# Optimization experiments

Hardware: AMD Instinct MI355X
Metric: run time of the kernel (lower is better)

Reference implementation:

```python
import jax, jax.numpy as jnp
import numpy as np

B, S, H = 8, 1024, 768
NUM_HEADS, DH = 12, 64
A, T = 12, 64

def setup_inputs() -> dict:
    key = jax.random.key(0)
    ks = jax.random.split(key, 12)
    all_tokens = jax.random.normal(ks[0], (B, S, H), dtype=jnp.float32)
    aspect_tokens = jax.random.normal(ks[1], (B, A, H), dtype=jnp.float32)
    # ragged target slices: start in [0, S-17), length in [1, 16]
    starts = jax.random.randint(ks[2], (T,), 0, S - 17)
    lens = jax.random.randint(ks[3], (T,), 1, 17)
    target_pos_info = jnp.stack([starts, starts + lens], axis=-1).astype(jnp.int32)  # (T,2)
    target_batch_info = jnp.sort(jax.random.randint(ks[4], (T,), 0, B)).astype(jnp.int32)
    attention_mask = jnp.ones((B, S), dtype=jnp.int32)
    s = 0.02
    W1 = jax.random.normal(ks[5], (H, H), dtype=jnp.float32) * s
    b1 = jnp.zeros((H,), dtype=jnp.float32)
    Wq = jax.random.normal(ks[6], (H, NUM_HEADS, DH), dtype=jnp.float32) * s
    bq = jnp.zeros((NUM_HEADS, DH), dtype=jnp.float32)
    Wk = jax.random.normal(ks[7], (H, NUM_HEADS, DH), dtype=jnp.float32) * s
    bk = jnp.zeros((NUM_HEADS, DH), dtype=jnp.float32)
    Wc = jax.random.normal(ks[8], (2 * H, 1), dtype=jnp.float32) * s
    bc = jnp.zeros((1,), dtype=jnp.float32)
    return {"all_tokens": all_tokens, "aspect_tokens": aspect_tokens,
            "target_pos_info": target_pos_info, "target_batch_info": target_batch_info,
            "attention_mask": attention_mask,
            "W1": W1, "b1": b1, "Wq": Wq, "bq": bq, "Wk": Wk, "bk": bk,
            "Wc": Wc, "bc": bc}


def reference(all_tokens, aspect_tokens, target_pos_info, target_batch_info,
              attention_mask, W1, b1, Wq, bq, Wk, bk, Wc, bc):
    # linear_transform (shared for tokens and aspects), dropout = identity at eval
    h = jax.nn.relu(jnp.einsum('bsh,hg->bsg', all_tokens, W1) + b1)     # (B,S,H)
    # SelfAttention: q/k EinsumDense projections; value = raw key_states reshaped
    q = jnp.einsum('bsh,hkd->bskd', h, Wq) + bq                          # (B,S,K,D)
    k = jnp.einsum('bsh,hkd->bskd', h, Wk) + bk
    v = h.reshape(k.shape)                                               # faithful: reshape, no proj
    q = q * jax.lax.rsqrt(jnp.asarray(DH, q.dtype))
    scores = jnp.einsum('bskd,bqkd->bkqs', k, q)                         # (B,K,Q,S)
    mask_val = attention_mask[:, 0].astype(scores.dtype)                 # original uses mask[:, 0:1]
    scores = scores + ((1.0 - mask_val) * -10000.0)[:, None, None, None]
    probs = jax.nn.softmax(scores, axis=-1)
    out = jnp.einsum('bkqs,bskd->bqkd', probs, v).reshape(h.shape)       # (B,S,H)
    # ragged per-target slice mean: masked mean over positions [s0, s1)
    pos = jnp.arange(S)
    s0, s1 = target_pos_info[:, 0], target_pos_info[:, 1]
    span = ((pos[None, :] >= s0[:, None]) & (pos[None, :] < s1[:, None])).astype(out.dtype)  # (T,S)
    gathered = out[target_batch_info]                                    # (T,S,H)
    counts = jnp.maximum(span.sum(-1, keepdims=True), 1.0)
    rep = jnp.einsum('ts,tsh->th', span, gathered) / counts              # (T,H)
    # aspect hidden states and target-aspect pairing (batch-ordered concat)
    h_a = jax.nn.relu(jnp.einsum('bah,hg->bag', aspect_tokens, W1) + b1)  # (B,A,H)
    pair = jnp.concatenate([jnp.broadcast_to(rep[:, None, :], (rep.shape[0], A, H)),
                            h_a[target_batch_info]], axis=-1)             # (T,A,2H)
    t_a_logit = jnp.einsum('tac,co->tao', pair, Wc) + bc                  # (T,A,1)
    return t_a_logit
```

## Files before the change

### kernel.cpp

```cpp
#include <hip/hip_runtime.h>


typedef __attribute__((ext_vector_type(8))) short s8v;
typedef __attribute__((ext_vector_type(4))) short s4v;
typedef __attribute__((ext_vector_type(4))) float f4v;

#define AS1 __attribute__((address_space(1)))
#define AS3 __attribute__((address_space(3)))

__device__ __forceinline__ unsigned short f2bf(float f) {
  union { float f; unsigned u; } v; v.f = f;
  unsigned r = v.u + 0x7FFFu + ((v.u >> 16) & 1u);
  return (unsigned short)(r >> 16);
}

__device__ __forceinline__ float bf2f(unsigned short u) {
  union { unsigned u; float f; } v; v.u = ((unsigned)u) << 16;
  return v.f;
}

__device__ __forceinline__ void gl2lds16(const void* g, void* l) {
  __builtin_amdgcn_global_load_lds((const AS1 void*)g, (AS3 void*)l, 16, 0, 0);
}

__global__ __launch_bounds__(256) void k_prep(const float* __restrict__ asp,
                                              const float* __restrict__ W1,
                                              const float* __restrict__ Wq,
                                              const float* __restrict__ Wk,
                                              unsigned short* __restrict__ Abf,
                                              unsigned short* __restrict__ W1t,
                                              unsigned short* __restrict__ Wqt,
                                              unsigned short* __restrict__ Wkt,
                                              float* __restrict__ outz) {
  __shared__ float T[64][68];
  int bid = blockIdx.x;
  int tid = threadIdx.x;
  if (bid < 36) {
    int i = bid * 256 + tid;
    const float4* src = (const float4*)(asp + (size_t)i * 8);
    float4 a = src[0], b = src[1];
    s8v o;
    o[0] = (short)f2bf(a.x); o[1] = (short)f2bf(a.y);
    o[2] = (short)f2bf(a.z); o[3] = (short)f2bf(a.w);
    o[4] = (short)f2bf(b.x); o[5] = (short)f2bf(b.y);
    o[6] = (short)f2bf(b.z); o[7] = (short)f2bf(b.w);
    *(s8v*)(Abf + (size_t)i * 8) = o;
  } else if (bid < 468) {
    int wb = bid - 36;
    const float* W = (wb < 144) ? W1 : (wb < 288) ? Wq : Wk;
    unsigned short* Wt = (wb < 144) ? W1t : (wb < 288) ? Wqt : Wkt;
    int tile = wb % 144;
    int tr = (tile / 12) * 64;
    int tc = (tile % 12) * 64;
#pragma unroll
    for (int p = 0; p < 4; ++p) {
      int r = p * 16 + (tid >> 4);
      int c = (tid & 15) * 4;
      float4 v = *(const float4*)(W + (size_t)(tr + r) * 768 + tc + c);
      T[r][c] = v.x; T[r][c + 1] = v.y; T[r][c + 2] = v.z; T[r][c + 3] = v.w;
    }
    __syncthreads();
#pragma unroll
    for (int p = 0; p < 2; ++p) {
      int n = p * 32 + (tid >> 3);
      int k8 = (tid & 7) * 8;
      s8v o;
#pragma unroll
      for (int j = 0; j < 8; ++j) o[j] = (short)f2bf(T[k8 + j][n]);
      *(s8v*)(Wt + (size_t)(tc + n) * 768 + tr + k8) = o;
    }
  } else {
#pragma unroll
    for (int q = 0; q < 3; ++q) outz[tid + q * 256] = 0.f;
  }
}

template <int MODE, bool AF32>
__device__ __forceinline__ void gemm_tile(int m0, int n0,
    const unsigned short* __restrict__ A, const float* __restrict__ Af,
    const unsigned short* __restrict__ Bt,
    const float* __restrict__ bias, unsigned short* __restrict__ C,
    unsigned short* __restrict__ C2, const int* __restrict__ pos,
    const int* __restrict__ tbi, unsigned short* As, unsigned short* Bs,
    int* srcRow) {
  const int K = 768;
  int tid = threadIdx.x, lane = tid & 63, w = tid >> 6;

  if (MODE == 2) {
    if (tid < 64) {
      int r = m0 + tid;
      int t = r >> 4, j = r & 15;
      int s0 = pos[2 * t], s1 = pos[2 * t + 1];
      int s = s0 + j; if (s > s1 - 1) s = s1 - 1;
      srcRow[tid] = tbi[t] * 1024 + s;
    }
    __syncthreads();
  }

  int rsub = lane >> 3;
  int cXor = ((lane & 7) ^ rsub) * 8;
  const unsigned short* aSrc[2];
  const float* aSrcF[2];
  const unsigned short* bSrc[4];
#pragma unroll
  for (int i = 0; i < 2; ++i) {
    int lr = (w * 2 + i) * 8 + rsub;
    size_t grow;
    if (MODE == 2) grow = (size_t)srcRow[lr];
    else if (MODE == 3) { int rr = m0 + lr; grow = (size_t)(rr < 96 ? rr : 95); }
    else grow = (size_t)(m0 + lr);
    if (AF32) aSrcF[i] = Af + grow * K + cXor;
    else aSrc[i] = A + grow * K + cXor;
  }
#pragma unroll
  for (int i = 0; i < 4; ++i) {
    int lr = (w * 4 + i) * 8 + rsub;
    bSrc[i] = Bt + (size_t)(n0 + lr) * K + cXor;
  }

  f4v acc[2][4];
#pragma unroll
  for (int i = 0; i < 2; ++i)
#pragma unroll
    for (int j = 0; j < 4; ++j) acc[i][j] = (f4v)(0.0f);

  int wm = (w >> 1) * 32, wn = (w & 1) * 64;
  int lc = lane & 15, lg = lane >> 4;
  int aIdx[2][2], bIdx[4][2];
#pragma unroll
  for (int mi = 0; mi < 2; ++mi) {
    int ra = wm + mi * 16 + lc;
#pragma unroll
    for (int kk = 0; kk < 2; ++kk)
      aIdx[mi][kk] = ra * 64 + (((kk * 4 + lg) ^ (ra & 7)) * 8);
  }
#pragma unroll
  for (int ni = 0; ni < 4; ++ni) {
    int rb = wn + ni * 16 + lc;
#pragma unroll
    for (int kk = 0; kk < 2; ++kk)
      bIdx[ni][kk] = rb * 64 + (((kk * 4 + lg) ^ (rb & 7)) * 8);
  }

  for (int k0 = 0; k0 < K; k0 += 64) {
#pragma unroll
    for (int i = 0; i < 4; ++i) gl2lds16(bSrc[i] + k0, Bs + (w * 4 + i) * 512);
    if (AF32) {
#pragma unroll
      for (int i = 0; i < 2; ++i) {
        const float* p = aSrcF[i] + k0;
        float4 v0 = *(const float4*)p;
        float4 v1 = *(const float4*)(p + 4);
        s8v o;
        o[0] = (short)f2bf(v0.x); o[1] = (short)f2bf(v0.y);
        o[2] = (short)f2bf(v0.z); o[3] = (short)f2bf(v0.w);
        o[4] = (short)f2bf(v1.x); o[5] = (short)f2bf(v1.y);
        o[6] = (short)f2bf(v1.z); o[7] = (short)f2bf(v1.w);
        *(s8v*)(As + (w * 2 + i) * 512 + lane * 8) = o;
      }
    } else {
#pragma unroll
      for (int i = 0; i < 2; ++i) gl2lds16(aSrc[i] + k0, As + (w * 2 + i) * 512);
    }
    __syncthreads();
#pragma unroll
    for (int kk = 0; kk < 2; ++kk) {
      s8v ar[2], br[4];
#pragma unroll
      for (int mi = 0; mi < 2; ++mi) ar[mi] = *(const s8v*)(As + aIdx[mi][kk]);
#pragma unroll
      for (int ni = 0; ni < 4; ++ni) br[ni] = *(const s8v*)(Bs + bIdx[ni][kk]);
#pragma unroll
      for (int mi = 0; mi < 2; ++mi)
#pragma unroll
        for (int ni = 0; ni < 4; ++ni)
          acc[mi][ni] = __builtin_amdgcn_mfma_f32_16x16x32_bf16(ar[mi], br[ni], acc[mi][ni], 0, 0, 0);
    }
    __syncthreads();
  }

#pragma unroll
  for (int mi = 0; mi < 2; ++mi) {
#pragma unroll
    for (int ni = 0; ni < 4; ++ni) {
      int col = n0 + wn + ni * 16 + lc;
      float bv = bias[col];
      int row0 = m0 + wm + mi * 16 + lg * 4;
      if (MODE == 0) {
        s4v pk;
#pragma unroll
        for (int r = 0; r < 4; ++r) {
          float x = acc[mi][ni][r] + bv;
          x = x > 0.f ? x : 0.f;
          unsigned short h = f2bf(x);
          pk[r] = (short)h;
          C[(size_t)(row0 + r) * 768 + col] = h;
        }
        int b = row0 >> 10, s = row0 & 1023;
        int kh = col >> 6, d = col & 63;
        *(s4v*)(C2 + ((size_t)((b * 12 + kh) * 64 + d)) * 1024 + s) = pk;
      } else if (MODE == 1) {
#pragma unroll
        for (int r = 0; r < 4; ++r) {
          int row = row0 + r;
          float x = acc[mi][ni][r] + bv;
          int b = row >> 10, s = row & 1023;
          int kh = col >> 6, d = col & 63;
          C[(size_t)((b * 12 + kh) * 1024 + s) * 64 + d] = f2bf(x);
        }
      } else if (MODE == 2) {
#pragma unroll
        for (int r = 0; r < 4; ++r) {
          int row = row0 + r;
          float x = (acc[mi][ni][r] + bv) * 0.125f;
          int t = row >> 4, j = row & 15;
          int kh = col >> 6, d = col & 63;
          C[(size_t)((t * 12 + kh) * 16 + j) * 64 + d] = f2bf(x);
        }
      } else {
#pragma unroll
        for (int r = 0; r < 4; ++r) {
          int row = row0 + r;
          float x = acc[mi][ni][r] + bv;
          x = x > 0.f ? x : 0.f;
          if (row < 96) C[(size_t)row * 768 + col] = f2bf(x);
        }
      }
    }
  }
}

__global__ __launch_bounds__(256) void k_gemmA(const float* __restrict__ X,
                                               const float* __restrict__ asp,
                                               const unsigned short* __restrict__ W1t,
                                               const float* __restrict__ b1,
                                               unsigned short* __restrict__ Hbf,
                                               unsigned short* __restrict__ Vt,
                                               unsigned short* __restrict__ Ha) {
  __shared__ unsigned short As[64 * 64];
  __shared__ unsigned short Bs[128 * 64];
  __shared__ int srcRow[64];
  int bid = blockIdx.x;
  if (bid < 768) {
    bid = (bid & 7) * 96 + (bid >> 3);
    gemm_tile<0, true>((bid / 6) * 64, (bid % 6) * 128, (const unsigned short*)nullptr,
                       X, W1t, b1, Hbf, Vt, (const int*)nullptr, (const int*)nullptr,
                       As, Bs, srcRow);
  } else {
    int b2 = bid - 768;
    gemm_tile<3, true>((b2 / 6) * 64, (b2 % 6) * 128, (const unsigned short*)nullptr,
                       asp, W1t, b1, Ha, (unsigned short*)nullptr,
                       (const int*)nullptr, (const int*)nullptr, As, Bs, srcRow);
  }
}

__global__ __launch_bounds__(256) void k_gemmB(const unsigned short* __restrict__ Hbf,
                                               const unsigned short* __restrict__ Wkt,
                                               const float* __restrict__ bk,
                                               unsigned short* __restrict__ Khm,
                                               const unsigned short* __restrict__ Wqt,
                                               const float* __restrict__ bq,
                                               unsigned short* __restrict__ Qhm,
                                               const int* __restrict__ pos,
                                               const int* __restrict__ tbi) {
  __shared__ unsigned short As[64 * 64];
  __shared__ unsigned short Bs[128 * 64];
  __shared__ int srcRow[64];
  int bid = blockIdx.x;
  bid = (bid & 7) * 108 + (bid >> 3);
  if (bid < 768) {
    gemm_tile<1, false>((bid / 6) * 64, (bid % 6) * 128, Hbf, (const float*)nullptr,
                        Wkt, bk, Khm, (unsigned short*)nullptr,
                        (const int*)nullptr, (const int*)nullptr, As, Bs, srcRow);
  } else {
    int b2 = bid - 768;
    gemm_tile<2, false>((b2 / 6) * 64, (b2 % 6) * 128, Hbf, (const float*)nullptr,
                        Wqt, bq, Qhm, (unsigned short*)nullptr, pos, tbi,
                        As, Bs, srcRow);
  }
}

__global__ __launch_bounds__(256) void k_attn(const unsigned short* __restrict__ q_hm,
                                              const unsigned short* __restrict__ k_hm,
                                              const unsigned short* __restrict__ vt,
                                              const unsigned short* __restrict__ ha,
                                              const int* __restrict__ pos,
                                              const int* __restrict__ tbi,
                                              const float* __restrict__ Wc,
                                              const float* __restrict__ bc,
                                              float* __restrict__ outp) {
  __shared__ unsigned short P[16 * 1032];
  __shared__ float O[4][16][64];
  __shared__ float rsbuf[4][16];
  __shared__ float inv_rs[16];
  __shared__ float hpart[4];
  __shared__ float rabuf;

  int bid = blockIdx.x;
  bid = (bid & 7) * 96 + (bid >> 3);
  int t = bid / 12, kh = bid % 12;
  int b = tbi[t];
  int s0 = pos[2 * t], s1 = pos[2 * t + 1];
  int len = s1 - s0;
  int tid = threadIdx.x, lane = tid & 63, w = tid >> 6;
  int lg = lane >> 4, lc = lane & 15;

  const unsigned short* qb = q_hm + (size_t)((t * 12 + kh) * 16) * 64;
  s8v a0 = *(const s8v*)(qb + (size_t)lc * 64 + lg * 8);
  s8v a1 = *(const s8v*)(qb + (size_t)lc * 64 + 32 + lg * 8);

  const unsigned short* kb = k_hm + (size_t)((b * 12 + kh) * 1024) * 64;
  float rs[4] = {0.f, 0.f, 0.f, 0.f};
  for (int it = 0; it < 16; ++it) {
    int sb = it * 64 + w * 16;
    s8v b0 = *(const s8v*)(kb + (size_t)(sb + lc) * 64 + lg * 8);
    s8v b1 = *(const s8v*)(kb + (size_t)(sb + lc) * 64 + 32 + lg * 8);
    f4v c = (f4v)(0.0f);
    c = __builtin_amdgcn_mfma_f32_16x16x32_bf16(a0, b0, c, 0, 0, 0);
    c = __builtin_amdgcn_mfma_f32_16x16x32_bf16(a1, b1, c, 0, 0, 0);
#pragma unroll
    for (int r = 0; r < 4; ++r) {
      float p = __expf(c[r]);
      rs[r] += p;
      P[(lg * 4 + r) * 1032 + sb + lc] = f2bf(p);
    }
  }
#pragma unroll
  for (int m = 1; m < 16; m <<= 1) {
#pragma unroll
    for (int r = 0; r < 4; ++r) rs[r] += __shfl_xor(rs[r], m, 64);
  }
  if (lc == 0) {
#pragma unroll
    for (int r = 0; r < 4; ++r) rsbuf[w][lg * 4 + r] = rs[r];
  }
  __syncthreads();
  if (tid < 16)
    inv_rs[tid] = 1.0f / (rsbuf[0][tid] + rsbuf[1][tid] + rsbuf[2][tid] + rsbuf[3][tid]);

  const unsigned short* vb = vt + (size_t)((b * 12 + kh) * 64) * 1024;
  f4v oc[4];
#pragma unroll
  for (int n = 0; n < 4; ++n) oc[n] = (f4v)(0.0f);
  for (int it = 0; it < 8; ++it) {
    int s32 = it * 128 + w * 32;
    s8v pa = *(const s8v*)(P + lc * 1032 + s32 + lg * 8);
#pragma unroll
    for (int n = 0; n < 4; ++n) {
      s8v vbf = *(const s8v*)(vb + (size_t)(n * 16 + lc) * 1024 + s32 + lg * 8);
      oc[n] = __builtin_amdgcn_mfma_f32_16x16x32_bf16(pa, vbf, oc[n], 0, 0, 0);
    }
  }
#pragma unroll
  for (int n = 0; n < 4; ++n)
#pragma unroll
    for (int r = 0; r < 4; ++r) O[w][lg * 4 + r][n * 16 + lc] = oc[n][r];
  __syncthreads();
  if (w == 0) {
    float sum = 0.f;
    for (int j = 0; j < len; ++j) {
      float v = O[0][j][lane] + O[1][j][lane] + O[2][j][lane] + O[3][j][lane];
      sum += v * inv_rs[j];
    }
    float repd = sum / (float)len;
    float pr = repd * Wc[kh * 64 + lane];
#pragma unroll
    for (int m = 1; m < 64; m <<= 1) pr += __shfl_xor(pr, m, 64);
    if (lane == 0) rabuf = pr;
  } else {
    const unsigned short* hr = ha + (size_t)(b * 12 + kh) * 768;
    float p2 = 0.f;
#pragma unroll
    for (int q = 0; q < 4; ++q) {
      int g = (tid - 64) + q * 192;
      p2 += bf2f(hr[g]) * Wc[768 + g];
    }
#pragma unroll
    for (int m = 1; m < 64; m <<= 1) p2 += __shfl_xor(p2, m, 64);
    if (lane == 0) hpart[w] = p2;
  }
  __syncthreads();
  if (tid < 12) {
    float ra = rabuf;
    float had = hpart[1] + hpart[2] + hpart[3];
    float v = ra + ((tid == kh) ? (had + bc[0]) : 0.f);
    atomicAdd(&outp[t * 12 + tid], v);
  }
}

extern "C" void kernel_launch(void* const* d_in, const int* in_sizes, int n_in,
                              void* d_out, int out_size, void* d_ws, size_t ws_size,
                              hipStream_t stream) {
  const float* all_tokens = (const float*)d_in[0];
  const float* aspect     = (const float*)d_in[1];
  const int*   pos        = (const int*)d_in[2];
  const int*   tbi        = (const int*)d_in[3];
  const float* W1 = (const float*)d_in[5];
  const float* b1 = (const float*)d_in[6];
  const float* Wq = (const float*)d_in[7];
  const float* bq = (const float*)d_in[8];
  const float* Wk = (const float*)d_in[9];
  const float* bk = (const float*)d_in[10];
  const float* Wc = (const float*)d_in[11];
  const float* bc = (const float*)d_in[12];
  float* out = (float*)d_out;

  char* ws = (char*)d_ws;
  unsigned short* W1t = (unsigned short*)(ws + 12582912);
  unsigned short* Wqt = (unsigned short*)(ws + 13762560);
  unsigned short* Wkt = (unsigned short*)(ws + 14942208);
  unsigned short* Hbf = (unsigned short*)(ws + 16121856);
  unsigned short* Khm = (unsigned short*)(ws + 28704768);
  unsigned short* Vt  = (unsigned short*)(ws + 41287680);
  unsigned short* Qhm = (unsigned short*)(ws + 53870592);
  unsigned short* Abf = (unsigned short*)(ws + 55640448);
  unsigned short* Ha  = (unsigned short*)(ws + 55787904);

  hipLaunchKernelGGL(k_prep, dim3(469), dim3(256), 0, stream,
                     aspect, W1, Wq, Wk, Abf, W1t, Wqt, Wkt, out);
  hipLaunchKernelGGL(k_gemmA, dim3(780), dim3(256), 0, stream,
                     all_tokens, aspect, W1t, b1, Hbf, Vt, Ha);
  hipLaunchKernelGGL(k_gemmB, dim3(864), dim3(256), 0, stream,
                     Hbf, Wkt, bk, Khm, Wqt, bq, Qhm, pos, tbi);
  hipLaunchKernelGGL(k_attn, dim3(768), dim3(256), 0, stream,
                     Qhm, Khm, Vt, Ha, pos, tbi, Wc, bc, out);
}
```

Measured before the change: 79.85 us.

## Pre-pack weights in MFMA fragment order and load B directly to registers

The weight-prep kernel now writes the bf16 weights in a packed layout that matches the MFMA B-operand fragment, tiled by 16 columns and 32 k-values. The GEMM tile reads its B fragments straight from global memory into registers, removing the B shared-memory buffer and its LDS traffic. This lowers LDS use, which may raise occupancy. In exchange, each wave loads B from global or L2 on its own instead of sharing a staged copy, and those loads are not overlapped by software beyond the barrier.

```diff
diff --git a/kernel.cpp b/kernel.cpp
--- a/kernel.cpp
+++ b/kernel.cpp
@@ -60,14 +60,18 @@
       T[r][c] = v.x; T[r][c + 1] = v.y; T[r][c + 2] = v.z; T[r][c + 3] = v.w;
     }
     __syncthreads();
+    int lane = tid & 63;
+    int ntl = tid >> 6;
+    int n_l = (ntl << 4) + (lane & 15);
+    int ntile = (tc >> 4) + ntl;
 #pragma unroll
     for (int p = 0; p < 2; ++p) {
-      int n = p * 32 + (tid >> 3);
-      int k8 = (tid & 7) * 8;
+      int k_l = p * 32 + (lane >> 4) * 8;
+      int kc = (tr >> 5) + p;
       s8v o;
 #pragma unroll
-      for (int j = 0; j < 8; ++j) o[j] = (short)f2bf(T[k8 + j][n]);
-      *(s8v*)(Wt + (size_t)(tc + n) * 768 + tr + k8) = o;
+      for (int j = 0; j < 8; ++j) o[j] = (short)f2bf(T[k_l + j][n_l]);
+      *(s8v*)(Wt + ((size_t)(ntile * 24 + kc) * 64 + lane) * 8) = o;
     }
   } else {
 #pragma unroll
@@ -78,11 +82,10 @@
 template <int MODE, bool AF32>
 __device__ __forceinline__ void gemm_tile(int m0, int n0,
     const unsigned short* __restrict__ A, const float* __restrict__ Af,
-    const unsigned short* __restrict__ Bt,
+    const unsigned short* __restrict__ Bfr,
     const float* __restrict__ bias, unsigned short* __restrict__ C,
     unsigned short* __restrict__ C2, const int* __restrict__ pos,
-    const int* __restrict__ tbi, unsigned short* As, unsigned short* Bs,
-    int* srcRow) {
+    const int* __restrict__ tbi, unsigned short* As, int* srcRow) {
   const int K = 768;
   int tid = threadIdx.x, lane = tid & 63, w = tid >> 6;
 
@@ -101,7 +104,6 @@
   int cXor = ((lane & 7) ^ rsub) * 8;
   const unsigned short* aSrc[2];
   const float* aSrcF[2];
-  const unsigned short* bSrc[4];
 #pragma unroll
   for (int i = 0; i < 2; ++i) {
     int lr = (w * 2 + i) * 8 + rsub;
@@ -112,11 +114,6 @@
     if (AF32) aSrcF[i] = Af + grow * K + cXor;
     else aSrc[i] = A + grow * K + cXor;
   }
-#pragma unroll
-  for (int i = 0; i < 4; ++i) {
-    int lr = (w * 4 + i) * 8 + rsub;
-    bSrc[i] = Bt + (size_t)(n0 + lr) * K + cXor;
-  }
 
   f4v acc[2][4];
 #pragma unroll
@@ -126,7 +123,7 @@
 
   int wm = (w >> 1) * 32, wn = (w & 1) * 64;
   int lc = lane & 15, lg = lane >> 4;
-  int aIdx[2][2], bIdx[4][2];
+  int aIdx[2][2];
 #pragma unroll
   for (int mi = 0; mi < 2; ++mi) {
     int ra = wm + mi * 16 + lc;
@@ -134,17 +131,15 @@
     for (int kk = 0; kk < 2; ++kk)
       aIdx[mi][kk] = ra * 64 + (((kk * 4 + lg) ^ (ra & 7)) * 8);
   }
+  const unsigned short* bBase[4];
 #pragma unroll
   for (int ni = 0; ni < 4; ++ni) {
-    int rb = wn + ni * 16 + lc;
-#pragma unroll
-    for (int kk = 0; kk < 2; ++kk)
-      bIdx[ni][kk] = rb * 64 + (((kk * 4 + lg) ^ (rb & 7)) * 8);
+    int ntile = ((n0 + wn) >> 4) + ni;
+    bBase[ni] = Bfr + ((size_t)ntile * 24 * 64 + lane) * 8;
   }
 
   for (int k0 = 0; k0 < K; k0 += 64) {
-#pragma unroll
-    for (int i = 0; i < 4; ++i) gl2lds16(bSrc[i] + k0, Bs + (w * 4 + i) * 512);
+    int ks = k0 >> 5;
     if (AF32) {
 #pragma unroll
       for (int i = 0; i < 2; ++i) {
@@ -162,19 +157,23 @@
 #pragma unroll
       for (int i = 0; i < 2; ++i) gl2lds16(aSrc[i] + k0, As + (w * 2 + i) * 512);
     }
+    s8v bf[2][4];
+#pragma unroll
+    for (int kk = 0; kk < 2; ++kk)
+#pragma unroll
+      for (int ni = 0; ni < 4; ++ni)
+        bf[kk][ni] = *(const s8v*)(bBase[ni] + (size_t)(ks + kk) * 512);
     __syncthreads();
 #pragma unroll
     for (int kk = 0; kk < 2; ++kk) {
-      s8v ar[2], br[4];
+      s8v ar[2];
 #pragma unroll
       for (int mi = 0; mi < 2; ++mi) ar[mi] = *(const s8v*)(As + aIdx[mi][kk]);
 #pragma unroll
-      for (int ni = 0; ni < 4; ++ni) br[ni] = *(const s8v*)(Bs + bIdx[ni][kk]);
-#pragma unroll
       for (int mi = 0; mi < 2; ++mi)
 #pragma unroll
         for (int ni = 0; ni < 4; ++ni)
-          acc[mi][ni] = __builtin_amdgcn_mfma_f32_16x16x32_bf16(ar[mi], br[ni], acc[mi][ni], 0, 0, 0);
+          acc[mi][ni] = __builtin_amdgcn_mfma_f32_16x16x32_bf16(ar[mi], bf[kk][ni], acc[mi][ni], 0, 0, 0);
     }
     __syncthreads();
   }
@@ -238,19 +237,18 @@
                                                unsigned short* __restrict__ Vt,
                                                unsigned short* __restrict__ Ha) {
   __shared__ unsigned short As[64 * 64];
-  __shared__ unsigned short Bs[128 * 64];
   __shared__ int srcRow[64];
   int bid = blockIdx.x;
   if (bid < 768) {
     bid = (bid & 7) * 96 + (bid >> 3);
     gemm_tile<0, true>((bid / 6) * 64, (bid % 6) * 128, (const unsigned short*)nullptr,
                        X, W1t, b1, Hbf, Vt, (const int*)nullptr, (const int*)nullptr,
-                       As, Bs, srcRow);
+                       As, srcRow);
   } else {
     int b2 = bid - 768;
     gemm_tile<3, true>((b2 / 6) * 64, (b2 % 6) * 128, (const unsigned short*)nullptr,
                        asp, W1t, b1, Ha, (unsigned short*)nullptr,
-                       (const int*)nullptr, (const int*)nullptr, As, Bs, srcRow);
+                       (const int*)nullptr, (const int*)nullptr, As, srcRow);
   }
 }
 
@@ -264,19 +262,18 @@
                                                const int* __restrict__ pos,
                                                const int* __restrict__ tbi) {
   __shared__ unsigned short As[64 * 64];
-  __shared__ unsigned short Bs[128 * 64];
   __shared__ int srcRow[64];
   int bid = blockIdx.x;
   bid = (bid & 7) * 108 + (bid >> 3);
   if (bid < 768) {
     gemm_tile<1, false>((bid / 6) * 64, (bid % 6) * 128, Hbf, (const float*)nullptr,
                         Wkt, bk, Khm, (unsigned short*)nullptr,
-                        (const int*)nullptr, (const int*)nullptr, As, Bs, srcRow);
+                        (const int*)nullptr, (const int*)nullptr, As, srcRow);
   } else {
     int b2 = bid - 768;
     gemm_tile<2, false>((b2 / 6) * 64, (b2 % 6) * 128, Hbf, (const float*)nullptr,
                         Wqt, bq, Qhm, (unsigned short*)nullptr, pos, tbi,
-                        As, Bs, srcRow);
+                        As, srcRow);
   }
 }
 
```

New measurement: 91.55 us. 1.15x slower.
